# Performance work log

Measured on AMD Instinct MI355X. Metric: run time of the kernel, lower is better.

Reference implementation:

```python
import jax, jax.numpy as jnp
import numpy as np

SIDE = 28
ROW_P = 0.1
BAND_WIDTH = 2
SEG_DROP_P = 0.8
HEAD_RATIO = 0.5


def _row_segment_mask(key, batch, side, band_width, row_p, drop_p):
    """Vectorized equivalent of _generate_row_segment_mask -> (batch, side*side) float mask."""
    k_row, k_start, k_drop = jax.random.split(key, 3)
    row_sel = jax.random.uniform(k_row, (batch, side)) < row_p  # row selected for dropout
    max_start = max(0, side - band_width)
    start = jax.random.randint(k_start, (batch, side), 0, max_start + 1)  # band start per row
    drop = jax.random.uniform(k_drop, (batch, side, band_width)) < drop_p  # per-col drop in band
    cols = jnp.arange(side)
    off = cols[None, None, :] - start[:, :, None]  # (batch, side, side) offset into band
    in_band = (off >= 0) & (off < band_width)
    drop_at = jnp.take_along_axis(drop, jnp.clip(off, 0, band_width - 1), axis=-1)
    dropped = row_sel[:, :, None] & in_band & drop_at  # (batch, side, side)
    return jnp.where(dropped, 0.0, 1.0).reshape(batch, side * side)


def _build_mask(key, batch, num_heads, seq_len, dtype):
    expected = SIDE * SIDE
    num_special = seq_len - expected  # leading special tokens (e.g. CLS)
    k_perm, k_masks = jax.random.split(key)
    num_drop_heads = max(1, int(num_heads * HEAD_RATIO))
    head_idx = jax.random.permutation(k_perm, num_heads)[:num_drop_heads]
    head_keys = jax.random.split(k_masks, num_drop_heads)
    head_masks = jax.vmap(
        lambda k: _row_segment_mask(k, batch, SIDE, BAND_WIDTH, ROW_P, SEG_DROP_P)
    )(head_keys)  # (num_drop_heads, batch, expected)
    full = jnp.ones((batch, num_heads, expected), dtype=dtype)
    full = full.at[:, head_idx, :].set(jnp.transpose(head_masks, (1, 0, 2)).astype(dtype))
    if num_special > 0:
        full = jnp.concatenate(
            [jnp.ones((batch, num_heads, num_special), dtype=dtype), full], axis=2
        )
    return full[..., None]  # (batch, num_heads, seq_len, 1)


def setup_inputs() -> dict:
    key = jax.random.key(0)
    v = jax.random.normal(key, (32, 16, 785, 64), dtype=jnp.float32)
    return {"v": v}


def reference(v) -> jnp.ndarray:
    batch, num_heads, seq_len, _ = v.shape
    mask = _build_mask(jax.random.key(42), batch, num_heads, seq_len, v.dtype)
    return v * mask
```

## Files before the change

### kernel.cpp

```cpp
#include <hip/hip_runtime.h>
#include <stdint.h>


struct U2 { uint32_t x, y; };

__device__ __forceinline__ uint32_t rotl32(uint32_t v, int r) {
    return (v << r) | (v >> (32 - r));
}

__device__ U2 threefry2x32(uint32_t k0, uint32_t k1, uint32_t c0, uint32_t c1) {
    uint32_t ks2 = k0 ^ k1 ^ 0x1BD11BDAu;
    uint32_t x0 = c0 + k0;
    uint32_t x1 = c1 + k1;
#define TF_RND(r) { x0 += x1; x1 = rotl32(x1, r); x1 ^= x0; }
    TF_RND(13) TF_RND(15) TF_RND(26) TF_RND(6)
    x0 += k1;  x1 += ks2 + 1u;
    TF_RND(17) TF_RND(29) TF_RND(16) TF_RND(24)
    x0 += ks2; x1 += k0 + 2u;
    TF_RND(13) TF_RND(15) TF_RND(26) TF_RND(6)
    x0 += k0;  x1 += k1 + 3u;
    TF_RND(17) TF_RND(29) TF_RND(16) TF_RND(24)
    x0 += k1;  x1 += ks2 + 4u;
    TF_RND(13) TF_RND(15) TF_RND(26) TF_RND(6)
    x0 += ks2; x1 += k0 + 5u;
#undef TF_RND
    U2 r; r.x = x0; r.y = x1; return r;
}

__device__ __forceinline__ U2 blk(U2 key, uint32_t i) {
    return threefry2x32(key.x, key.y, 0u, i);
}
__device__ __forceinline__ uint32_t rb32(U2 key, uint32_t i) {
    U2 b = blk(key, i);
    return b.x ^ b.y;
}
__device__ __forceinline__ float u01(uint32_t bits) {
    uint32_t fb = (bits >> 9) | 0x3f800000u;
    return __uint_as_float(fb) - 1.0f;
}

#define BATCH 32
#define NHEADS 16
#define SEQ 785
#define SIDE 28
#define NDROP 8
#define ROWS_PER_HEAD (BATCH * SIDE)
#define TOTAL_ROWS (NDROP * ROWS_PER_HEAD)

__global__ void __launch_bounds__(256)
copy_kernel(const float4* __restrict__ v, float4* __restrict__ out, int nvec) {
    int stride = gridDim.x * blockDim.x;
    for (int i = blockIdx.x * blockDim.x + threadIdx.x; i < nvec; i += stride) {
        out[i] = v[i];
    }
}

__global__ void __launch_bounds__(256)
zero_dropped_kernel(float* __restrict__ out) {
    __shared__ uint32_t lds_sk[NHEADS];
    __shared__ int lds_hidx[NDROP];

    const U2 base = {0u, 42u};

    if (threadIdx.x < NHEADS) {
        U2 k_perm  = blk(base, 0);
        U2 subkey  = blk(k_perm, 1);
        lds_sk[threadIdx.x] = rb32(subkey, threadIdx.x);
    }
    __syncthreads();
    if (threadIdx.x < NHEADS) {
        uint32_t mysk = lds_sk[threadIdx.x];
        int rank = 0;
        for (int i = 0; i < NHEADS; ++i)
            if (lds_sk[i] < mysk || (lds_sk[i] == mysk && i < (int)threadIdx.x)) ++rank;
        if (rank < NDROP) lds_hidx[rank] = (int)threadIdx.x;
    }
    __syncthreads();

    int t = blockIdx.x * blockDim.x + threadIdx.x;
    if (t >= TOTAL_ROWS) return;
    uint32_t j  = (uint32_t)t / ROWS_PER_HEAD;
    uint32_t br = (uint32_t)t % ROWS_PER_HEAD;

    U2 k_masks = blk(base, 1);
    U2 hk      = blk(k_masks, j);

    U2 k_row = blk(hk, 0);
    if (!(u01(rb32(k_row, br)) < 0.1f)) return;

    U2 k_start = blk(hk, 1);
    U2 k_drop  = blk(hk, 2);
    U2 kh = blk(k_start, 0);
    U2 kl = blk(k_start, 1);
    uint32_t hi = rb32(kh, br);
    uint32_t lo = rb32(kl, br);
    uint32_t start = ((hi % 27u) * 22u + (lo % 27u)) % 27u;

    uint32_t drop0 = (u01(rb32(k_drop, 2u * br))      < 0.8f) ? 1u : 0u;
    uint32_t drop1 = (u01(rb32(k_drop, 2u * br + 1u)) < 0.8f) ? 1u : 0u;
    if (!(drop0 | drop1)) return;

    uint32_t b = br / SIDE;
    uint32_t r = br % SIDE;
    uint32_t h = (uint32_t)lds_hidx[j];
    size_t rowbase = (((size_t)b * NHEADS + h) * SEQ + 1u + r * SIDE + start) * 64u;

    const float4 z = {0.f, 0.f, 0.f, 0.f};
    if (drop0) {
        float4* p = (float4*)(out + rowbase);
        #pragma unroll
        for (int q = 0; q < 16; ++q) p[q] = z;
    }
    if (drop1) {
        float4* p = (float4*)(out + rowbase + 64u);
        #pragma unroll
        for (int q = 0; q < 16; ++q) p[q] = z;
    }
}

extern "C" void kernel_launch(void* const* d_in, const int* in_sizes, int n_in,
                              void* d_out, int out_size, void* d_ws, size_t ws_size,
                              hipStream_t stream) {
    const float* v = (const float*)d_in[0];
    float* out = (float*)d_out;

    int nvec = out_size / 4;
    copy_kernel<<<2048, 256, 0, stream>>>(
        (const float4*)v, (float4*)out, nvec);

    zero_dropped_kernel<<<(TOTAL_ROWS + 255) / 256, 256, 0, stream>>>(out);
}
```

Before: 45.03 us.

## Fuse copy and dropout zeroing into one streaming multiply kernel

Replaces the separate copy kernel and scatter-zero kernel with a single kernel. Each block loads its slice of v into registers, computes one mask value per token into LDS by regenerating the threefry randomness, then multiplies and writes with nontemporal stores. This drops the second launch and the extra write pass over dropped rows, at the cost of per-token RNG work on up to 128 threads per block. The grid assumes the element count divides exactly into TPB*VPT float4 chunks (32*16*785*64/4 = 6,430,720 = 3140*2048, so it holds).

```diff
diff --git a/kernel.cpp b/kernel.cpp
--- a/kernel.cpp
+++ b/kernel.cpp
@@ -3,6 +3,8 @@
 
 
 struct U2 { uint32_t x, y; };
+
+typedef float f32x4 __attribute__((ext_vector_type(4)));
 
 __device__ __forceinline__ uint32_t rotl32(uint32_t v, int r) {
     return (v << r) | (v >> (32 - r));
@@ -44,27 +46,28 @@
 #define SEQ 785
 #define SIDE 28
 #define NDROP 8
-#define ROWS_PER_HEAD (BATCH * SIDE)
-#define TOTAL_ROWS (NDROP * ROWS_PER_HEAD)
 
-__global__ void __launch_bounds__(256)
-copy_kernel(const float4* __restrict__ v, float4* __restrict__ out, int nvec) {
-    int stride = gridDim.x * blockDim.x;
-    for (int i = blockIdx.x * blockDim.x + threadIdx.x; i < nvec; i += stride) {
-        out[i] = v[i];
-    }
-}
+#define VPT 8
+#define TPB 256
+#define TOK_PER_BLK ((TPB * VPT) / 16)
 
-__global__ void __launch_bounds__(256)
-zero_dropped_kernel(float* __restrict__ out) {
+__global__ void __launch_bounds__(TPB)
+fused_dropout_kernel(const f32x4* __restrict__ v, f32x4* __restrict__ out) {
     __shared__ uint32_t lds_sk[NHEADS];
-    __shared__ int lds_hidx[NDROP];
+    __shared__ int      lds_hm[NHEADS];
+    __shared__ float    lds_m[TOK_PER_BLK];
 
     const U2 base = {0u, 42u};
 
+    const int base4 = blockIdx.x * (TPB * VPT) + threadIdx.x;
+
+    f32x4 r[VPT];
+    #pragma unroll
+    for (int k = 0; k < VPT; ++k) r[k] = v[base4 + k * TPB];
+
     if (threadIdx.x < NHEADS) {
-        U2 k_perm  = blk(base, 0);
-        U2 subkey  = blk(k_perm, 1);
+        U2 k_perm = blk(base, 0);
+        U2 subkey = blk(k_perm, 1);
         lds_sk[threadIdx.x] = rb32(subkey, threadIdx.x);
     }
     __syncthreads();
@@ -73,48 +76,51 @@
         int rank = 0;
         for (int i = 0; i < NHEADS; ++i)
             if (lds_sk[i] < mysk || (lds_sk[i] == mysk && i < (int)threadIdx.x)) ++rank;
-        if (rank < NDROP) lds_hidx[rank] = (int)threadIdx.x;
+        lds_hm[threadIdx.x] = (rank < NDROP) ? rank : -1;
     }
     __syncthreads();
 
-    int t = blockIdx.x * blockDim.x + threadIdx.x;
-    if (t >= TOTAL_ROWS) return;
-    uint32_t j  = (uint32_t)t / ROWS_PER_HEAD;
-    uint32_t br = (uint32_t)t % ROWS_PER_HEAD;
+    if (threadIdx.x < TOK_PER_BLK) {
+        int tok = blockIdx.x * TOK_PER_BLK + threadIdx.x;
+        uint32_t s  = (uint32_t)tok % SEQ;
+        uint32_t bh = (uint32_t)tok / SEQ;
+        uint32_t h  = bh & (NHEADS - 1);
+        uint32_t b  = bh >> 4;
+        float m = 1.0f;
+        int j = lds_hm[h];
+        if (j >= 0 && s >= 1) {
+            uint32_t pos = s - 1;
+            uint32_t rr = pos / SIDE;
+            uint32_t c  = pos - rr * SIDE;
+            uint32_t br = b * SIDE + rr;
+            U2 k_masks = blk(base, 1);
+            U2 hk      = blk(k_masks, (uint32_t)j);
+            U2 k_row   = blk(hk, 0);
+            if (u01(rb32(k_row, br)) < 0.1f) {
+                U2 k_start = blk(hk, 1);
+                U2 kh = blk(k_start, 0);
+                U2 kl = blk(k_start, 1);
+                uint32_t hi = rb32(kh, br);
+                uint32_t lo = rb32(kl, br);
+                uint32_t start = ((hi % 27u) * 22u + (lo % 27u)) % 27u;
+                int off = (int)c - (int)start;
+                if (off >= 0 && off < 2) {
+                    U2 k_drop = blk(hk, 2);
+                    if (u01(rb32(k_drop, 2u * br + (uint32_t)off)) < 0.8f)
+                        m = 0.0f;
+                }
+            }
+        }
+        lds_m[threadIdx.x] = m;
+    }
+    __syncthreads();
 
-    U2 k_masks = blk(base, 1);
-    U2 hk      = blk(k_masks, j);
-
-    U2 k_row = blk(hk, 0);
-    if (!(u01(rb32(k_row, br)) < 0.1f)) return;
-
-    U2 k_start = blk(hk, 1);
-    U2 k_drop  = blk(hk, 2);
-    U2 kh = blk(k_start, 0);
-    U2 kl = blk(k_start, 1);
-    uint32_t hi = rb32(kh, br);
-    uint32_t lo = rb32(kl, br);
-    uint32_t start = ((hi % 27u) * 22u + (lo % 27u)) % 27u;
-
-    uint32_t drop0 = (u01(rb32(k_drop, 2u * br))      < 0.8f) ? 1u : 0u;
-    uint32_t drop1 = (u01(rb32(k_drop, 2u * br + 1u)) < 0.8f) ? 1u : 0u;
-    if (!(drop0 | drop1)) return;
-
-    uint32_t b = br / SIDE;
-    uint32_t r = br % SIDE;
-    uint32_t h = (uint32_t)lds_hidx[j];
-    size_t rowbase = (((size_t)b * NHEADS + h) * SEQ + 1u + r * SIDE + start) * 64u;
-
-    const float4 z = {0.f, 0.f, 0.f, 0.f};
-    if (drop0) {
-        float4* p = (float4*)(out + rowbase);
-        #pragma unroll
-        for (int q = 0; q < 16; ++q) p[q] = z;
-    }
-    if (drop1) {
-        float4* p = (float4*)(out + rowbase + 64u);
-        #pragma unroll
-        for (int q = 0; q < 16; ++q) p[q] = z;
+    #pragma unroll
+    for (int k = 0; k < VPT; ++k) {
+        int i4 = threadIdx.x + k * TPB;
+        float m = lds_m[i4 >> 4];
+        r[k] *= m;
+        __builtin_nontemporal_store(r[k], &out[base4 + k * TPB]);
     }
 }
 
@@ -125,8 +131,7 @@
     float* out = (float*)d_out;
 
     int nvec = out_size / 4;
-    copy_kernel<<<2048, 256, 0, stream>>>(
-        (const float4*)v, (float4*)out, nvec);
-
-    zero_dropped_kernel<<<(TOTAL_ROWS + 255) / 256, 256, 0, stream>>>(out);
+    int blocks = nvec / (TPB * VPT);
+    fused_dropout_kernel<<<blocks, TPB, 0, stream>>>(
+        (const f32x4*)v, (f32x4*)out);
 }
```

After: 36.61 us, median of 2. 18.7% less time.
